# Performance work log

Measured on AMD Instinct MI355X. Metric: run time of the kernel, lower is better.

## Reference

```python
import jax, jax.numpy as jnp
import numpy as np

N, K, C_IN, OUT = 65536, 16, 64, 64
MID = OUT  # mid_planes = out_planes // 1
S = 8      # share_planes
EPS = 1e-5


def _bn(x, gamma, beta, mean, var):
    # Keras BatchNormalization (inference) over the last (channel) axis.
    return (x - mean) * jax.lax.rsqrt(var + EPS) * gamma + beta


def setup_inputs() -> dict:
    key = jax.random.key(0)
    ks = jax.random.split(key, 12)
    d = {
        'point': jax.random.normal(ks[0], (N, 3), jnp.float32),
        'feat': jax.random.normal(ks[1], (N, C_IN), jnp.float32),
        'idx': jax.random.randint(ks[2], (N, K), 0, N, jnp.int32),
        # linear_q / linear_k / linear_v
        'Wq': jax.random.normal(ks[3], (C_IN, MID), jnp.float32) * 0.05,
        'bq': jnp.zeros((MID,), jnp.float32),
        'Wk': jax.random.normal(ks[4], (C_IN, MID), jnp.float32) * 0.05,
        'bk': jnp.zeros((MID,), jnp.float32),
        'Wv': jax.random.normal(ks[5], (C_IN, OUT), jnp.float32) * 0.05,
        'bv': jnp.zeros((OUT,), jnp.float32),
        # linear_p: Dense(3) -> BN -> ReLU -> Dense(out)
        'p_w1': jax.random.normal(ks[6], (3, 3), jnp.float32) * 0.5,
        'p_b1': jnp.zeros((3,), jnp.float32),
        'p_bn_g': jnp.ones((3,), jnp.float32),
        'p_bn_b': jnp.zeros((3,), jnp.float32),
        'p_bn_m': jnp.zeros((3,), jnp.float32),
        'p_bn_v': jnp.ones((3,), jnp.float32),
        'p_w2': jax.random.normal(ks[7], (3, OUT), jnp.float32) * 0.1,
        'p_b2': jnp.zeros((OUT,), jnp.float32),
        # linear_w: BN -> ReLU -> Dense(mid//s) -> BN -> ReLU -> Dense(out//s)
        'w_bn1_g': jnp.ones((MID,), jnp.float32),
        'w_bn1_b': jnp.zeros((MID,), jnp.float32),
        'w_bn1_m': jnp.zeros((MID,), jnp.float32),
        'w_bn1_v': jnp.ones((MID,), jnp.float32),
        'w_w1': jax.random.normal(ks[8], (MID, MID // S), jnp.float32) * 0.05,
        'w_b1': jnp.zeros((MID // S,), jnp.float32),
        'w_bn2_g': jnp.ones((MID // S,), jnp.float32),
        'w_bn2_b': jnp.zeros((MID // S,), jnp.float32),
        'w_bn2_m': jnp.zeros((MID // S,), jnp.float32),
        'w_bn2_v': jnp.ones((MID // S,), jnp.float32),
        'w_w2': jax.random.normal(ks[9], (MID // S, OUT // S), jnp.float32) * 0.1,
        'w_b2': jnp.zeros((OUT // S,), jnp.float32),
    }
    return d


def reference(point, feat, idx, Wq, bq, Wk, bk, Wv, bv,
              p_w1, p_b1, p_bn_g, p_bn_b, p_bn_m, p_bn_v, p_w2, p_b2,
              w_bn1_g, w_bn1_b, w_bn1_m, w_bn1_v, w_w1, w_b1,
              w_bn2_g, w_bn2_b, w_bn2_m, w_bn2_v, w_w2, w_b2):
    n = point.shape[0]
    feat_q = feat @ Wq + bq                       # (n, mid)
    feat_k = feat @ Wk + bk                       # (n, mid)
    feat_v = feat @ Wv + bv                       # (n, out)
    # queryandgroup: KNN gather + relative positions
    g_xyz = point[idx] - point[:, None, :]        # (n, k, 3)
    g_k = feat_k[idx]                             # (n, k, mid)
    g_v = feat_v[idx]                             # (n, k, out)
    # linear_p MLP on relative positions
    p = g_xyz @ p_w1 + p_b1
    p = jax.nn.relu(_bn(p, p_bn_g, p_bn_b, p_bn_m, p_bn_v))
    p = p @ p_w2 + p_b2                           # (n, k, out)
    # sum over out_planes//mid_planes (= 1) groups, kept for faithfulness
    pr = p.reshape(n, K, OUT // MID, MID).sum(axis=2)  # (n, k, mid)
    # subtraction attention scores
    w = g_k - feat_q[:, None, :] + pr             # (n, k, mid)
    w = jax.nn.relu(_bn(w, w_bn1_g, w_bn1_b, w_bn1_m, w_bn1_v))
    w = w @ w_w1 + w_b1                           # (n, k, mid//s)
    w = jax.nn.relu(_bn(w, w_bn2_g, w_bn2_b, w_bn2_m, w_bn2_v))
    w = w @ w_w2 + w_b2                           # (n, k, out//s)
    # NOTE: original uses Softmax(axis=-1) -> over the out//share channel axis
    w = jax.nn.softmax(w, axis=-1)
    # grouped weighted sum over neighbors
    v = (g_v + p).reshape(n, K, S, OUT // S)      # (n, k, s, out//s)
    out = (v * w[:, :, None, :]).sum(axis=1)      # (n, s, out//s)
    return out.reshape(n, OUT)
```

## Files before the change

kernel.cpp:

```cpp
#include <hip/hip_runtime.h>

typedef unsigned short u16;
typedef unsigned int   u32;
typedef float f32x2 __attribute__((ext_vector_type(2)));

__device__ __forceinline__ u16 f2b(float f) {
    u32 u = __float_as_uint(f);
    return (u16)((u + 0x7fffu + ((u >> 16) & 1u)) >> 16);
}
__device__ __forceinline__ u32 pack2f(float a, float b) {
    return (u32)f2b(a) | ((u32)f2b(b) << 16);
}
__device__ __forceinline__ f32x2 unpk2(u32 w) {
    f32x2 r;
    r[0] = __uint_as_float(w << 16);
    r[1] = __uint_as_float(w & 0xffff0000u);
    return r;
}
__device__ __forceinline__ int permc(int c) { return ((c & 7) << 3) | (c >> 3); }
__device__ __forceinline__ f32x2 bc2(float x) { f32x2 r; r[0] = x; r[1] = x; return r; }
__device__ __forceinline__ f32x2 mk2(float a, float b) { f32x2 r; r[0] = a; r[1] = b; return r; }

__device__ __forceinline__ void dot2bf(float& c, u32 a, u32 b) {
    asm("v_dot2_f32_bf16 %0, %1, %2, %0" : "+v"(c) : "v"(a), "v"(b));
}
__device__ __forceinline__ u32 cvtpk(float lo, float hi) {
    u32 r;
    asm("v_cvt_pk_bf16_f32 %0, %1, %2" : "=v"(r) : "v"(lo), "v"(hi));
    return r;
}

template<int CTRL>
__device__ __forceinline__ float dppf(float x) {
    return __int_as_float(__builtin_amdgcn_update_dpp(0, __float_as_int(x), CTRL, 0xf, 0xf, true));
}
__device__ __forceinline__ float gsum8(float x) {
    x += dppf<0xB1>(x);
    x += dppf<0x4E>(x);
    x += dppf<0x141>(x);
    return x;
}
__device__ __forceinline__ float gmax8(float x) {
    x = fmaxf(x, dppf<0xB1>(x));
    x = fmaxf(x, dppf<0x4E>(x));
    x = fmaxf(x, dppf<0x141>(x));
    return x;
}
__device__ __forceinline__ int phi8(int r) { return (r < 4) ? r : (r ^ 3); }

__global__ __launch_bounds__(256) void qkv_kernel(
    const float* __restrict__ feat,
    const float* __restrict__ Wq, const float* __restrict__ bq,
    const float* __restrict__ Wk, const float* __restrict__ bk,
    const float* __restrict__ Wv, const float* __restrict__ bv,
    u16* __restrict__ qt, u16* __restrict__ kvt)
{
    __shared__ u32 wpk[3][32][64];
    __shared__ u32 fpk[32][132];
    const int t = threadIdx.x;
    const int rowbase = blockIdx.x * 128;

    {
        const float* Ws[3] = {Wq, Wk, Wv};
#pragma unroll
        for (int mm = 0; mm < 3; mm++) {
            for (int e = t; e < 512; e += 256) {
                int ip = e >> 4, c4 = (e & 15) * 4;
                float4 wa = *(const float4*)&Ws[mm][(2 * ip) * 64 + c4];
                float4 wb = *(const float4*)&Ws[mm][(2 * ip + 1) * 64 + c4];
                wpk[mm][ip][permc(c4 + 0)] = pack2f(wa.x, wb.x);
                wpk[mm][ip][permc(c4 + 1)] = pack2f(wa.y, wb.y);
                wpk[mm][ip][permc(c4 + 2)] = pack2f(wa.z, wb.z);
                wpk[mm][ip][permc(c4 + 3)] = pack2f(wa.w, wb.w);
            }
        }
    }
    for (int e = t; e < 2048; e += 256) {
        int r = e >> 4, ip2 = (e & 15) * 2;
        float4 v = *(const float4*)&feat[(size_t)(rowbase + r) * 64 + ip2 * 2];
        fpk[ip2][r]     = pack2f(v.x, v.y);
        fpk[ip2 + 1][r] = pack2f(v.z, v.w);
    }
    __syncthreads();

    const int rg = t >> 3;
    const int q8 = t & 7;
    const int c0 = q8 * 8;

    float acc[3][4][8];
    {
        const float* Bs[3] = {bq, bk, bv};
#pragma unroll
        for (int m = 0; m < 3; m++)
#pragma unroll
            for (int x = 0; x < 8; x++) {
                float b = Bs[m][x * 8 + q8];
#pragma unroll
                for (int r = 0; r < 4; r++) acc[m][r][x] = b;
            }
    }

#pragma unroll 2
    for (int ip = 0; ip < 32; ip++) {
        uint4 f4 = *(const uint4*)&fpk[ip][rg * 4];
        u32 fr[4] = {f4.x, f4.y, f4.z, f4.w};
#pragma unroll
        for (int m = 0; m < 3; m++) {
            uint4 wv0 = *(const uint4*)&wpk[m][ip][c0];
            uint4 wv1 = *(const uint4*)&wpk[m][ip][c0 + 4];
            u32 wc[8] = {wv0.x, wv0.y, wv0.z, wv0.w, wv1.x, wv1.y, wv1.z, wv1.w};
#pragma unroll
            for (int r = 0; r < 4; r++)
#pragma unroll
                for (int x = 0; x < 8; x++)
                    dot2bf(acc[m][r][x], fr[r], wc[x]);
        }
    }

#pragma unroll
    for (int r = 0; r < 4; r++) {
        int row = rowbase + rg * 4 + r;
        uint4 oq, ok, ov;
        oq.x = cvtpk(acc[0][r][0], acc[0][r][1]); oq.y = cvtpk(acc[0][r][2], acc[0][r][3]);
        oq.z = cvtpk(acc[0][r][4], acc[0][r][5]); oq.w = cvtpk(acc[0][r][6], acc[0][r][7]);
        ok.x = cvtpk(acc[1][r][0], acc[1][r][1]); ok.y = cvtpk(acc[1][r][2], acc[1][r][3]);
        ok.z = cvtpk(acc[1][r][4], acc[1][r][5]); ok.w = cvtpk(acc[1][r][6], acc[1][r][7]);
        ov.x = cvtpk(acc[2][r][0], acc[2][r][1]); ov.y = cvtpk(acc[2][r][2], acc[2][r][3]);
        ov.z = cvtpk(acc[2][r][4], acc[2][r][5]); ov.w = cvtpk(acc[2][r][6], acc[2][r][7]);
        *(uint4*)&qt [(size_t)row * 64 + c0]       = oq;
        *(uint4*)&kvt[(size_t)row * 128 + c0]      = ok;
        *(uint4*)&kvt[(size_t)row * 128 + 64 + c0] = ov;
    }
}

__global__ __launch_bounds__(256) void attn_kernel(
    const float* __restrict__ point,
    const int*   __restrict__ idx,
    const u16*   __restrict__ qt,
    const u16*   __restrict__ kvt,
    const float* __restrict__ p_w1,   const float* __restrict__ p_b1,
    const float* __restrict__ p_bn_g, const float* __restrict__ p_bn_b,
    const float* __restrict__ p_bn_m, const float* __restrict__ p_bn_v,
    const float* __restrict__ p_w2,   const float* __restrict__ p_b2,
    const float* __restrict__ w_bn1_g, const float* __restrict__ w_bn1_b,
    const float* __restrict__ w_bn1_m, const float* __restrict__ w_bn1_v,
    const float* __restrict__ w_w1,    const float* __restrict__ w_b1,
    const float* __restrict__ w_bn2_g, const float* __restrict__ w_bn2_b,
    const float* __restrict__ w_bn2_m, const float* __restrict__ w_bn2_v,
    const float* __restrict__ w_w2,    const float* __restrict__ w_b2,
    float* __restrict__ out)
{
    const int t  = threadIdx.x;
    const int l8 = t & 7;
    const int n  = blockIdx.x * 32 + (t >> 3);
    const float EPS = 1e-5f;

    float pw1[9];
#pragma unroll
    for (int i = 0; i < 9; i++) pw1[i] = p_w1[i];
    float pb1b[3], pbs[3], pbh[3];
#pragma unroll
    for (int a = 0; a < 3; a++) {
        float s = p_bn_g[a] * rsqrtf(p_bn_v[a] + EPS);
        pb1b[a] = p_b1[a];
        pbs[a]  = s;
        pbh[a]  = p_bn_b[a] - p_bn_m[a] * s;
    }

    f32x2 P0[4], P1[4], P2[4], PB[4];
#pragma unroll
    for (int p = 0; p < 4; p++) {
        int ce = 16 * p + l8, co = ce + 8;
        P0[p] = mk2(p_w2[ce],       p_w2[co]);
        P1[p] = mk2(p_w2[64 + ce],  p_w2[64 + co]);
        P2[p] = mk2(p_w2[128 + ce], p_w2[128 + co]);
        PB[p] = mk2(p_b2[ce],       p_b2[co]);
    }
    u32 W1pk[4][8];
#pragma unroll
    for (int p = 0; p < 4; p++) {
        int ce = 16 * p + l8, co = ce + 8;
#pragma unroll
        for (int r = 0; r < 8; r++) {
            int hh = phi8(r) ^ l8;
            W1pk[p][r] = pack2f(w_w1[ce * 8 + hh], w_w1[co * 8 + hh]);
        }
    }
    float b2s_l, b2hh_l;
    {
        float s = w_bn2_g[l8] * rsqrtf(w_bn2_v[l8] + EPS);
        b2s_l  = s;
        b2hh_l = (w_bn2_b[l8] - w_bn2_m[l8] * s) + w_b1[l8] * s;
    }
    u32 ww2xpk[4];
#pragma unroll
    for (int i = 0; i < 4; i++) {
        int h0 = phi8(2 * i)     ^ l8;
        int h1 = phi8(2 * i + 1) ^ l8;
        ww2xpk[i] = pack2f(w_w2[h0 * 8 + l8], w_w2[h1 * 8 + l8]);
    }
    const float wb2l = w_b2[l8];

    f32x2 s2[4], qh2[4];
    {
        uint4 qr = *(const uint4*)&qt[(size_t)n * 64 + l8 * 8];
        const u32* qw = (const u32*)&qr;
#pragma unroll
        for (int p = 0; p < 4; p++) {
            int ce = 16 * p + l8, co = ce + 8;
            float se = w_bn1_g[ce] * rsqrtf(w_bn1_v[ce] + EPS);
            float so = w_bn1_g[co] * rsqrtf(w_bn1_v[co] + EPS);
            float he = w_bn1_b[ce] - w_bn1_m[ce] * se;
            float ho = w_bn1_b[co] - w_bn1_m[co] * so;
            f32x2 q2 = unpk2(qw[p]);
            s2[p]  = mk2(se, so);
            qh2[p] = mk2(he - q2[0] * se, ho - q2[1] * so);
        }
    }

    const float px = point[n * 3], py = point[n * 3 + 1], pz = point[n * 3 + 2];
    f32x2 acc2[4];
#pragma unroll
    for (int p = 0; p < 4; p++) acc2[p] = mk2(0.f, 0.f);

    uint4 kr, vr;
    float2 jxy;
    float  jz;

    auto proc = [&](int jn) {
        const u16* kpn = kvt + (size_t)jn * 128 + l8 * 8;
        uint4 krn = *(const uint4*)kpn;
        uint4 vrn = *(const uint4*)(kpn + 64);
        float2 jxyn = *(const float2*)&point[jn * 3];
        float  jzn  = point[jn * 3 + 2];

        float dx = jxy.x - px, dy = jxy.y - py, dz = jz - pz;
        float t0 = fmaxf(0.f, fmaf(fmaf(dz, pw1[6], fmaf(dy, pw1[3], fmaf(dx, pw1[0], pb1b[0]))), pbs[0], pbh[0]));
        float t1 = fmaxf(0.f, fmaf(fmaf(dz, pw1[7], fmaf(dy, pw1[4], fmaf(dx, pw1[1], pb1b[1]))), pbs[1], pbh[1]));
        float t2 = fmaxf(0.f, fmaf(fmaf(dz, pw1[8], fmaf(dy, pw1[5], fmaf(dx, pw1[2], pb1b[2]))), pbs[2], pbh[2]));
        f32x2 tp0 = bc2(t0), tp1 = bc2(t1), tp2 = bc2(t2);

        const u32* kw = (const u32*)&kr;
        float part[8];
#pragma unroll
        for (int h = 0; h < 8; h++) part[h] = 0.f;
        f32x2 pjs[4];

#pragma unroll
        for (int p = 0; p < 4; p++) {
            f32x2 pj = PB[p] + tp0 * P0[p] + tp1 * P1[p] + tp2 * P2[p];
            pjs[p] = pj;
            f32x2 kf = unpk2(kw[p]);
            f32x2 w2 = (kf + pj) * s2[p] + qh2[p];
            u32 wpk_ = cvtpk(fmaxf(w2[0], 0.f), fmaxf(w2[1], 0.f));
#pragma unroll
            for (int r = 0; r < 8; r++) dot2bf(part[r], wpk_, W1pk[p][r]);
        }
        part[0] += dppf<0xB1>(part[1]);
        part[2] += dppf<0xB1>(part[3]);
        part[4] += dppf<0xB1>(part[5]);
        part[6] += dppf<0xB1>(part[7]);
        part[0] += dppf<0x4E>(part[2]);
        part[4] += dppf<0x4E>(part[6]);
        part[0] += dppf<0x141>(part[4]);
        float wbl = fmaxf(0.f, fmaf(part[0], b2s_l, b2hh_l));
        float u1 = dppf<0xB1>(wbl);
        float u2 = dppf<0x4E>(wbl);
        float u3 = dppf<0x4E>(u1);
        float u4 = dppf<0x141>(wbl);
        float u5 = dppf<0x141>(u1);
        float u6 = dppf<0x141>(u2);
        float u7 = dppf<0x141>(u3);
        float y = wb2l;
        dot2bf(y, cvtpk(wbl, u1), ww2xpk[0]);
        dot2bf(y, cvtpk(u2, u3), ww2xpk[1]);
        dot2bf(y, cvtpk(u4, u5), ww2xpk[2]);
        dot2bf(y, cvtpk(u6, u7), ww2xpk[3]);

        float mx = gmax8(y);
        float e  = __expf(y - mx);
        float ssum = gsum8(e);
        float sm = e * __builtin_amdgcn_rcpf(ssum);
        f32x2 sm2 = bc2(sm);

        const u32* vw = (const u32*)&vr;
#pragma unroll
        for (int p = 0; p < 4; p++) {
            f32x2 vp = unpk2(vw[p]) + pjs[p];
            acc2[p] += sm2 * vp;
        }

        kr = krn; vr = vrn; jxy = jxyn; jz = jzn;
    };

    const int4* idxq = (const int4*)(idx + n * 16);
    int4 I = idxq[0];
    {
        const u16* kp0 = kvt + (size_t)I.x * 128 + l8 * 8;
        kr  = *(const uint4*)kp0;
        vr  = *(const uint4*)(kp0 + 64);
        jxy = *(const float2*)&point[I.x * 3];
        jz  = point[I.x * 3 + 2];
    }
#pragma unroll
    for (int kg = 0; kg < 4; kg++) {
        int4 In = (kg < 3) ? idxq[kg + 1] : I;
        proc(I.y);
        proc(I.z);
        proc(I.w);
        proc(In.x);
        I = In;
    }

#pragma unroll
    for (int p = 0; p < 4; p++) {
        out[(size_t)n * 64 + 16 * p + l8]     = acc2[p][0];
        out[(size_t)n * 64 + 16 * p + 8 + l8] = acc2[p][1];
    }
}

extern "C" void kernel_launch(void* const* d_in, const int* in_sizes, int n_in,
                              void* d_out, int out_size, void* d_ws, size_t ws_size,
                              hipStream_t stream)
{
    const float* point   = (const float*)d_in[0];
    const float* feat    = (const float*)d_in[1];
    const int*   idx     = (const int*)d_in[2];
    const float* Wq      = (const float*)d_in[3];
    const float* bq      = (const float*)d_in[4];
    const float* Wk      = (const float*)d_in[5];
    const float* bk      = (const float*)d_in[6];
    const float* Wv      = (const float*)d_in[7];
    const float* bv      = (const float*)d_in[8];
    const float* p_w1    = (const float*)d_in[9];
    const float* p_b1    = (const float*)d_in[10];
    const float* p_bn_g  = (const float*)d_in[11];
    const float* p_bn_b  = (const float*)d_in[12];
    const float* p_bn_m  = (const float*)d_in[13];
    const float* p_bn_v  = (const float*)d_in[14];
    const float* p_w2    = (const float*)d_in[15];
    const float* p_b2    = (const float*)d_in[16];
    const float* w_bn1_g = (const float*)d_in[17];
    const float* w_bn1_b = (const float*)d_in[18];
    const float* w_bn1_m = (const float*)d_in[19];
    const float* w_bn1_v = (const float*)d_in[20];
    const float* w_w1    = (const float*)d_in[21];
    const float* w_b1    = (const float*)d_in[22];
    const float* w_bn2_g = (const float*)d_in[23];
    const float* w_bn2_b = (const float*)d_in[24];
    const float* w_bn2_m = (const float*)d_in[25];
    const float* w_bn2_v = (const float*)d_in[26];
    const float* w_w2    = (const float*)d_in[27];
    const float* w_b2    = (const float*)d_in[28];
    float* out = (float*)d_out;

    const int N = in_sizes[0] / 3;

    u16* kvt = (u16*)d_ws;
    u16* qt  = (u16*)d_ws + (size_t)N * 128;

    qkv_kernel<<<N / 128, 256, 0, stream>>>(feat, Wq, bq, Wk, bk, Wv, bv, qt, kvt);
    attn_kernel<<<N / 32, 256, 0, stream>>>(point, idx, qt, kvt,
                                            p_w1, p_b1, p_bn_g, p_bn_b, p_bn_m, p_bn_v, p_w2, p_b2,
                                            w_bn1_g, w_bn1_b, w_bn1_m, w_bn1_v, w_w1, w_b1,
                                            w_bn2_g, w_bn2_b, w_bn2_m, w_bn2_v, w_w2, w_b2,
                                            out);
}
```

Baseline: 83.34 us.

## Deepen neighbor gather prefetch to two stages and use packed f32 FMA asm

Loads all 16 neighbor indices up front and prefetches the key, value and point data for the neighbor two iterations ahead instead of one, so more gather latency is hidden behind compute. It also replaces scalar and vector f32 arithmetic with explicit v_pk_fma_f32 and v_pk_add_f32 inline asm, including pairing two of the three position-MLP channels. The deeper prefetch raises register pressure by one extra set of buffers, which could lower occupancy. The inline asm blocks the compiler from scheduling or fusing those operations itself.

```diff
diff --git a/kernel.cpp b/kernel.cpp
--- a/kernel.cpp
+++ b/kernel.cpp
@@ -21,6 +21,14 @@
 __device__ __forceinline__ f32x2 bc2(float x) { f32x2 r; r[0] = x; r[1] = x; return r; }
 __device__ __forceinline__ f32x2 mk2(float a, float b) { f32x2 r; r[0] = a; r[1] = b; return r; }
 
+__device__ __forceinline__ void pk_fma(f32x2& d, f32x2 a, f32x2 b) {
+    asm("v_pk_fma_f32 %0, %1, %2, %0" : "+v"(d) : "v"(a), "v"(b));
+}
+__device__ __forceinline__ f32x2 pk_add(f32x2 a, f32x2 b) {
+    f32x2 d;
+    asm("v_pk_add_f32 %0, %1, %2" : "=v"(d) : "v"(a), "v"(b));
+    return d;
+}
 __device__ __forceinline__ void dot2bf(float& c, u32 a, u32 b) {
     asm("v_dot2_f32_bf16 %0, %1, %2, %0" : "+v"(c) : "v"(a), "v"(b));
 }
@@ -166,6 +174,12 @@
         pbs[a]  = s;
         pbh[a]  = p_bn_b[a] - p_bn_m[a] * s;
     }
+    f32x2 pw1p0 = mk2(pw1[0], pw1[1]);
+    f32x2 pw1p1 = mk2(pw1[3], pw1[4]);
+    f32x2 pw1p2 = mk2(pw1[6], pw1[7]);
+    f32x2 pb01  = mk2(pb1b[0], pb1b[1]);
+    f32x2 pbs01 = mk2(pbs[0], pbs[1]);
+    f32x2 pbh01 = mk2(pbh[0], pbh[1]);
 
     f32x2 P0[4], P1[4], P2[4], PB[4];
 #pragma unroll
@@ -223,24 +237,51 @@
 #pragma unroll
     for (int p = 0; p < 4; p++) acc2[p] = mk2(0.f, 0.f);
 
-    uint4 kr, vr;
-    float2 jxy;
-    float  jz;
-
-    auto proc = [&](int jn) {
-        const u16* kpn = kvt + (size_t)jn * 128 + l8 * 8;
-        uint4 krn = *(const uint4*)kpn;
-        uint4 vrn = *(const uint4*)(kpn + 64);
-        float2 jxyn = *(const float2*)&point[jn * 3];
-        float  jzn  = point[jn * 3 + 2];
-
-        float dx = jxy.x - px, dy = jxy.y - py, dz = jz - pz;
-        float t0 = fmaxf(0.f, fmaf(fmaf(dz, pw1[6], fmaf(dy, pw1[3], fmaf(dx, pw1[0], pb1b[0]))), pbs[0], pbh[0]));
-        float t1 = fmaxf(0.f, fmaf(fmaf(dz, pw1[7], fmaf(dy, pw1[4], fmaf(dx, pw1[1], pb1b[1]))), pbs[1], pbh[1]));
+    int js[16];
+    {
+        const int4* idxq = (const int4*)(idx + n * 16);
+        *(int4*)&js[0]  = idxq[0];
+        *(int4*)&js[4]  = idxq[1];
+        *(int4*)&js[8]  = idxq[2];
+        *(int4*)&js[12] = idxq[3];
+    }
+    uint4 kA, vA, kB, vB;
+    float2 xyA, xyB;
+    float  zA, zB;
+    {
+        const u16* kp0 = kvt + (size_t)js[0] * 128 + l8 * 8;
+        kA  = *(const uint4*)kp0;
+        vA  = *(const uint4*)(kp0 + 64);
+        xyA = *(const float2*)&point[js[0] * 3];
+        zA  = point[js[0] * 3 + 2];
+        const u16* kp1 = kvt + (size_t)js[1] * 128 + l8 * 8;
+        kB  = *(const uint4*)kp1;
+        vB  = *(const uint4*)(kp1 + 64);
+        xyB = *(const float2*)&point[js[1] * 3];
+        zB  = point[js[1] * 3 + 2];
+    }
+
+#pragma unroll
+    for (int i = 0; i < 16; i++) {
+        int jn = js[(i + 2 < 16) ? i + 2 : 15];
+        const u16* kp = kvt + (size_t)jn * 128 + l8 * 8;
+        uint4 kC  = *(const uint4*)kp;
+        uint4 vC  = *(const uint4*)(kp + 64);
+        float2 xyC = *(const float2*)&point[jn * 3];
+        float  zC  = point[jn * 3 + 2];
+
+        float dx = xyA.x - px, dy = xyA.y - py, dz = zA - pz;
+        f32x2 t01 = pb01;
+        pk_fma(t01, bc2(dx), pw1p0);
+        pk_fma(t01, bc2(dy), pw1p1);
+        pk_fma(t01, bc2(dz), pw1p2);
+        f32x2 tb = pbh01;
+        pk_fma(tb, t01, pbs01);
+        float t0 = fmaxf(tb[0], 0.f), t1 = fmaxf(tb[1], 0.f);
         float t2 = fmaxf(0.f, fmaf(fmaf(dz, pw1[8], fmaf(dy, pw1[5], fmaf(dx, pw1[2], pb1b[2]))), pbs[2], pbh[2]));
         f32x2 tp0 = bc2(t0), tp1 = bc2(t1), tp2 = bc2(t2);
 
-        const u32* kw = (const u32*)&kr;
+        const u32* kw = (const u32*)&kA;
         float part[8];
 #pragma unroll
         for (int h = 0; h < 8; h++) part[h] = 0.f;
@@ -248,10 +289,14 @@
 
 #pragma unroll
         for (int p = 0; p < 4; p++) {
-            f32x2 pj = PB[p] + tp0 * P0[p] + tp1 * P1[p] + tp2 * P2[p];
+            f32x2 pj = PB[p];
+            pk_fma(pj, tp0, P0[p]);
+            pk_fma(pj, tp1, P1[p]);
+            pk_fma(pj, tp2, P2[p]);
             pjs[p] = pj;
-            f32x2 kf = unpk2(kw[p]);
-            f32x2 w2 = (kf + pj) * s2[p] + qh2[p];
+            f32x2 kpj = pk_add(unpk2(kw[p]), pj);
+            f32x2 w2 = qh2[p];
+            pk_fma(w2, kpj, s2[p]);
             u32 wpk_ = cvtpk(fmaxf(w2[0], 0.f), fmaxf(w2[1], 0.f));
 #pragma unroll
             for (int r = 0; r < 8; r++) dot2bf(part[r], wpk_, W1pk[p][r]);
@@ -283,33 +328,15 @@
         float sm = e * __builtin_amdgcn_rcpf(ssum);
         f32x2 sm2 = bc2(sm);
 
-        const u32* vw = (const u32*)&vr;
+        const u32* vw = (const u32*)&vA;
 #pragma unroll
         for (int p = 0; p < 4; p++) {
-            f32x2 vp = unpk2(vw[p]) + pjs[p];
-            acc2[p] += sm2 * vp;
-        }
-
-        kr = krn; vr = vrn; jxy = jxyn; jz = jzn;
-    };
-
-    const int4* idxq = (const int4*)(idx + n * 16);
-    int4 I = idxq[0];
-    {
-        const u16* kp0 = kvt + (size_t)I.x * 128 + l8 * 8;
-        kr  = *(const uint4*)kp0;
-        vr  = *(const uint4*)(kp0 + 64);
-        jxy = *(const float2*)&point[I.x * 3];
-        jz  = point[I.x * 3 + 2];
-    }
-#pragma unroll
-    for (int kg = 0; kg < 4; kg++) {
-        int4 In = (kg < 3) ? idxq[kg + 1] : I;
-        proc(I.y);
-        proc(I.z);
-        proc(I.w);
-        proc(In.x);
-        I = In;
+            f32x2 vp = pk_add(unpk2(vw[p]), pjs[p]);
+            pk_fma(acc2[p], sm2, vp);
+        }
+
+        kA = kB; vA = vB; xyA = xyB; zA = zB;
+        kB = kC; vB = vC; xyB = xyC; zB = zC;
     }
 
 #pragma unroll
```

Measured after the change: 89.12 us. +6.9%, slower.
